# Kernel tuning notes

Measured on AMD Instinct MI355X. Metric: run time of the kernel, lower is better.

Reference implementation:

```python
import jax, jax.numpy as jnp
import numpy as np

B, T, D, FF, E = 4, 2048, 512, 2048, 8
TOP_K = 2
EPS = 0.01


def setup_inputs() -> dict:
    key = jax.random.key(0)
    ks = jax.random.split(key, 7)
    s = 0.02
    return {
        "x": jax.random.normal(ks[0], (B, T, D), dtype=jnp.float32),
        "Wg": jax.random.normal(ks[1], (D, E), dtype=jnp.float32) * s,
        "bg": jnp.zeros((E,), dtype=jnp.float32),
        "W1": jax.random.normal(ks[2], (E, D, FF), dtype=jnp.float32) * s,
        "b1": jnp.zeros((E, FF), dtype=jnp.float32),
        "W2": jax.random.normal(ks[3], (E, FF, D), dtype=jnp.float32) * s,
        "b2": jnp.zeros((E, D), dtype=jnp.float32),
    }


def reference(x, Wg, bg, W1, b1, W2, b2):
    b, t, d = x.shape
    e = Wg.shape[1]
    # Gating: softmax over experts, top-k selection, renormalize with eps.
    logits = jnp.einsum("btd,de->bte", x, Wg) + bg          # [B,T,E]
    gates = jax.nn.softmax(logits, axis=-1)
    vals, idx = jax.lax.top_k(gates, TOP_K)                  # [B,T,K]
    vals = vals / (jnp.sum(vals, axis=-1, keepdims=True) + EPS)
    # Per-token per-expert combine weight (scatter of top-k vals into E slots).
    w = jnp.sum(jax.nn.one_hot(idx, e, dtype=x.dtype) * vals[..., None], axis=-2)  # [B,T,E]
    w = w.reshape(-1, e)                                     # [N,E], N=B*T
    xf = x.reshape(-1, d)                                    # [N,D]
    # Per-expert FFN (Linear -> ReLU -> Linear); zero-weight tokens contribute 0,
    # matching the original's masked gather/scatter.
    h = jax.nn.relu(jnp.einsum("nd,edf->enf", xf, W1) + b1[:, None, :])  # [E,N,FF]
    y = jnp.einsum("enf,efd->end", h, W2) + b2[:, None, :]               # [E,N,D]
    out = jnp.einsum("ne,end->nd", w, y)                                 # [N,D]
    return out.reshape(b, t, d)
```

## Files before the change

kernel.cpp:

```cpp
#include <hip/hip_runtime.h>
#include <hip/hip_bf16.h>
#include <cstdint>

#define NTOK   8192
#define DDIM   512
#define FDIM   2048
#define NEXP   8
#define NSLOT  16384
#define MAXTILES 136

typedef __bf16 bf16;
typedef __bf16 bf16x8 __attribute__((ext_vector_type(8)));
typedef float  f32x4  __attribute__((ext_vector_type(4)));

typedef uint32_t __attribute__((address_space(1))) gu32;
typedef uint32_t __attribute__((address_space(3))) lu32;

__device__ __forceinline__ void gload16(const void* g, void* l) {
    __builtin_amdgcn_global_load_lds((const gu32*)(uintptr_t)g,
                                     (lu32*)(uintptr_t)l, 16, 0, 0);
}

__global__ __launch_bounds__(256)
void gating_kernel(const float* __restrict__ x, const float* __restrict__ Wg,
                   const float* __restrict__ bg, bf16* __restrict__ xb,
                   int* __restrict__ top_idx, float* __restrict__ top_w,
                   int* __restrict__ counts)
{
    __shared__ int cnt_s[NEXP];
    if (threadIdx.x < NEXP) cnt_s[threadIdx.x] = 0;
    __syncthreads();

    const int w = threadIdx.x >> 6;
    const int l = threadIdx.x & 63;
    const int gw = blockIdx.x * 4 + w;

    for (int n = gw; n < NTOK; n += 4096) {
        const float4* xp = (const float4*)(x + (size_t)n * DDIM + l * 8);
        float4 x0 = xp[0], x1 = xp[1];
        float xf[8] = {x0.x, x0.y, x0.z, x0.w, x1.x, x1.y, x1.z, x1.w};

        bf16x8 xv;
#pragma unroll
        for (int i = 0; i < 8; ++i) xv[i] = (bf16)xf[i];
        *(bf16x8*)(xb + (size_t)n * DDIM + l * 8) = xv;

        float acc[8] = {0.f,0.f,0.f,0.f,0.f,0.f,0.f,0.f};
#pragma unroll
        for (int i = 0; i < 8; ++i) {
            const float4* wp = (const float4*)(Wg + (size_t)(l * 8 + i) * NEXP);
            float4 wa = wp[0], wb = wp[1];
            acc[0] += xf[i] * wa.x; acc[1] += xf[i] * wa.y;
            acc[2] += xf[i] * wa.z; acc[3] += xf[i] * wa.w;
            acc[4] += xf[i] * wb.x; acc[5] += xf[i] * wb.y;
            acc[6] += xf[i] * wb.z; acc[7] += xf[i] * wb.w;
        }
#pragma unroll
        for (int m = 32; m >= 1; m >>= 1)
#pragma unroll
            for (int e = 0; e < 8; ++e)
                acc[e] += __shfl_xor(acc[e], m);

        if (l == 0) {
            float logit[8];
#pragma unroll
            for (int e = 0; e < 8; ++e) logit[e] = acc[e] + bg[e];
            float mx = logit[0];
#pragma unroll
            for (int e = 1; e < 8; ++e) mx = fmaxf(mx, logit[e]);
            float g[8], s = 0.f;
#pragma unroll
            for (int e = 0; e < 8; ++e) { g[e] = expf(logit[e] - mx); s += g[e]; }
            float inv = 1.f / s;
#pragma unroll
            for (int e = 0; e < 8; ++e) g[e] *= inv;
            int e0 = 0;
#pragma unroll
            for (int e = 1; e < 8; ++e) if (g[e] > g[e0]) e0 = e;
            int e1 = (e0 == 0) ? 1 : 0;
#pragma unroll
            for (int e = 0; e < 8; ++e) if (e != e0 && e != e1 && g[e] > g[e1]) e1 = e;
            float denom = g[e0] + g[e1] + 0.01f;
            top_idx[n * 2 + 0] = e0;
            top_idx[n * 2 + 1] = e1;
            top_w[n * 2 + 0] = g[e0] / denom;
            top_w[n * 2 + 1] = g[e1] / denom;
            atomicAdd(&cnt_s[e0], 1);
            atomicAdd(&cnt_s[e1], 1);
        }
    }
    __syncthreads();
    if (threadIdx.x < NEXP) atomicAdd(&counts[threadIdx.x], cnt_s[threadIdx.x]);
}

__global__ void scan_kernel(const int* __restrict__ counts, int* __restrict__ offsets,
                            int* __restrict__ tmap_e, int* __restrict__ tmap_rt,
                            int* __restrict__ ntiles, int* __restrict__ cursors)
{
    if (threadIdx.x == 0) {
        int off = 0;
        for (int e = 0; e < NEXP; ++e) { offsets[e] = off; off += counts[e]; cursors[e] = 0; }
        offsets[NEXP] = off;
        int t = 0;
        for (int e = 0; e < NEXP; ++e) {
            int nt = (counts[e] + 127) >> 7;
            for (int rt = 0; rt < nt; ++rt) { tmap_e[t] = e; tmap_rt[t] = rt; ++t; }
        }
        *ntiles = t;
    }
}

__global__ __launch_bounds__(256)
void scatter_kernel(const int* __restrict__ top_idx, const float* __restrict__ top_w,
                    const int* __restrict__ offsets, int* __restrict__ cursors,
                    int* __restrict__ slot_tok, float* __restrict__ slot_w,
                    int* __restrict__ pos)
{
    __shared__ int lcnt[NEXP];
    __shared__ int lbase[NEXP];
    const int t = threadIdx.x;
    if (t < NEXP) lcnt[t] = 0;
    __syncthreads();
    const int n = blockIdx.x * 256 + t;
    const int e0 = top_idx[n * 2 + 0];
    const int e1 = top_idx[n * 2 + 1];
    const int r0 = atomicAdd(&lcnt[e0], 1);
    const int r1 = atomicAdd(&lcnt[e1], 1);
    __syncthreads();
    if (t < NEXP) lbase[t] = atomicAdd(&cursors[t], lcnt[t]);
    __syncthreads();
    const int s0 = offsets[e0] + lbase[e0] + r0;
    const int s1 = offsets[e1] + lbase[e1] + r1;
    slot_tok[s0] = n; slot_w[s0] = top_w[n * 2 + 0]; pos[n * 2 + 0] = s0;
    slot_tok[s1] = n; slot_w[s1] = top_w[n * 2 + 1]; pos[n * 2 + 1] = s1;
}

__global__ __launch_bounds__(256)
void transpose_cvt(const float* __restrict__ src, bf16* __restrict__ dst, int R, int C)
{
    __shared__ bf16 tile[64][72];
    const size_t eo = (size_t)blockIdx.z * R * C;
    src += eo; dst += eo;
    const int c0 = blockIdx.x * 64, r0 = blockIdx.y * 64;
    const int tq = (threadIdx.x & 15) * 4;
    const int tr = threadIdx.x >> 4;
#pragma unroll
    for (int j = 0; j < 4; ++j) {
        const int r = tr + j * 16;
        float4 v = *(const float4*)(src + (size_t)(r0 + r) * C + c0 + tq);
        tile[tq + 0][r] = (bf16)v.x;
        tile[tq + 1][r] = (bf16)v.y;
        tile[tq + 2][r] = (bf16)v.z;
        tile[tq + 3][r] = (bf16)v.w;
    }
    __syncthreads();
    const int x8 = (threadIdx.x & 7) * 8;
    const int cr = threadIdx.x >> 3;
#pragma unroll
    for (int j = 0; j < 2; ++j) {
        const int c = cr + j * 32;
        *(bf16x8*)(dst + (size_t)(c0 + c) * R + r0 + x8) = *(const bf16x8*)&tile[c][x8];
    }
}

template<int KD, int ND, bool FIRST>
__global__ __launch_bounds__(512)
void moe_gemm(const bf16* __restrict__ Adata, const bf16* __restrict__ Bt,
              const float* __restrict__ bias, void* __restrict__ Out,
              const int* __restrict__ slot_tok, const int* __restrict__ offsets,
              const int* __restrict__ tmap_e, const int* __restrict__ tmap_rt,
              const int* __restrict__ ntiles)
{
    const int ty = blockIdx.y;
    if (ty >= *ntiles) return;
    const int e    = tmap_e[ty];
    const int rt   = tmap_rt[ty];
    const int row0 = offsets[e] + rt * 128;
    const int rowEnd = offsets[e + 1];
    const int nb   = blockIdx.x * 128;

    __shared__ __align__(16) bf16 As[4 * 128 * 32];
    __shared__ __align__(16) bf16 Bs[4 * 128 * 32];

    const int t = threadIdx.x;
    const int w = t >> 6, l = t & 63;
    const int wm = w >> 1, wn = w & 1;

    const int rA   = w * 16 + (l >> 2);
    const int colb = (l & 3) * 8;

    int srow = row0 + rA; if (srow >= NSLOT) srow = NSLOT - 1;
    const bf16* aSrc;
    if (FIRST) aSrc = Adata + (size_t)slot_tok[srow] * KD + colb;
    else       aSrc = Adata + (size_t)srow * KD + colb;
    const bf16* bSrc = Bt + ((size_t)e * ND + nb + rA) * KD + colb;

    const int offW = w * 512;

    f32x4 acc[2][4] = {};
    const int lr = l & 15;
    const int lk = (l >> 4) * 8;

    constexpr int NT = KD / 32;

    auto STAGE = [&](int buf, int k0) {
        gload16(aSrc + k0, As + buf * 4096 + offW);
        gload16(bSrc + k0, Bs + buf * 4096 + offW);
    };
    auto COMPUTE = [&](int buf) {
        const bf16* ab = As + buf * 4096;
        const bf16* bb = Bs + buf * 4096;
        bf16x8 aF[2], bF[4];
#pragma unroll
        for (int mi = 0; mi < 2; ++mi)
            aF[mi] = *(const bf16x8*)(ab + (wm * 32 + mi * 16 + lr) * 32 + lk);
#pragma unroll
        for (int nj = 0; nj < 4; ++nj)
            bF[nj] = *(const bf16x8*)(bb + (wn * 64 + nj * 16 + lr) * 32 + lk);
#pragma unroll
        for (int mi = 0; mi < 2; ++mi)
#pragma unroll
            for (int nj = 0; nj < 4; ++nj)
                acc[mi][nj] = __builtin_amdgcn_mfma_f32_16x16x32_bf16(
                    aF[mi], bF[nj], acc[mi][nj], 0, 0, 0);
    };

    STAGE(0, 0);
    STAGE(1, 32);
    STAGE(2, 64);
    STAGE(3, 96);
    __builtin_amdgcn_sched_barrier(0);

    for (int t2 = 0; t2 < NT - 4; ++t2) {
        asm volatile("s_waitcnt vmcnt(6)" ::: "memory");
        __builtin_amdgcn_sched_barrier(0);
        __builtin_amdgcn_s_barrier();
        __builtin_amdgcn_sched_barrier(0);
        COMPUTE(t2 & 3);
        __builtin_amdgcn_s_barrier();
        __builtin_amdgcn_sched_barrier(0);
        STAGE(t2 & 3, (t2 + 4) * 32);
        __builtin_amdgcn_sched_barrier(0);
    }
    asm volatile("s_waitcnt vmcnt(6)" ::: "memory");
    __builtin_amdgcn_sched_barrier(0);
    __builtin_amdgcn_s_barrier();
    __builtin_amdgcn_sched_barrier(0);
    COMPUTE((NT - 4) & 3);
    asm volatile("s_waitcnt vmcnt(4)" ::: "memory");
    __builtin_amdgcn_sched_barrier(0);
    __builtin_amdgcn_s_barrier();
    __builtin_amdgcn_sched_barrier(0);
    COMPUTE((NT - 3) & 3);
    asm volatile("s_waitcnt vmcnt(2)" ::: "memory");
    __builtin_amdgcn_sched_barrier(0);
    __builtin_amdgcn_s_barrier();
    __builtin_amdgcn_sched_barrier(0);
    COMPUTE((NT - 2) & 3);
    asm volatile("s_waitcnt vmcnt(0)" ::: "memory");
    __builtin_amdgcn_sched_barrier(0);
    __builtin_amdgcn_s_barrier();
    __builtin_amdgcn_sched_barrier(0);
    COMPUTE((NT - 1) & 3);

    const int rowW = row0 + wm * 32;
    const int colW = nb + wn * 64;
#pragma unroll
    for (int mi = 0; mi < 2; ++mi) {
#pragma unroll
        for (int nj = 0; nj < 4; ++nj) {
#pragma unroll
            for (int r = 0; r < 4; ++r) {
                int row = rowW + mi * 16 + (l >> 4) * 4 + r;
                int col = colW + nj * 16 + lr;
                if (row < rowEnd) {
                    float v = acc[mi][nj][r] + bias[e * ND + col];
                    if (FIRST)
                        ((bf16*)Out)[(size_t)row * ND + col] = (bf16)fmaxf(v, 0.f);
                    else
                        ((float*)Out)[(size_t)row * ND + col] = v;
                }
            }
        }
    }
}

__global__ __launch_bounds__(256)
void combine_kernel(const float* __restrict__ Yg, const int* __restrict__ pos,
                    const float* __restrict__ slot_w, float* __restrict__ out)
{
    int idx = blockIdx.x * 256 + threadIdx.x;
    int n = idx >> 7;
    int d4 = idx & 127;
    int s0 = pos[n * 2 + 0], s1 = pos[n * 2 + 1];
    float w0 = slot_w[s0], w1 = slot_w[s1];
    float4 a = ((const float4*)(Yg + (size_t)s0 * DDIM))[d4];
    float4 b = ((const float4*)(Yg + (size_t)s1 * DDIM))[d4];
    float4 o;
    o.x = w0 * a.x + w1 * b.x;
    o.y = w0 * a.y + w1 * b.y;
    o.z = w0 * a.z + w1 * b.z;
    o.w = w0 * a.w + w1 * b.w;
    ((float4*)out)[idx] = o;
}

extern "C" void kernel_launch(void* const* d_in, const int* in_sizes, int n_in,
                              void* d_out, int out_size, void* d_ws, size_t ws_size,
                              hipStream_t stream)
{
    (void)in_sizes; (void)n_in;
    const float* x  = (const float*)d_in[0];
    const float* Wg = (const float*)d_in[1];
    const float* bg = (const float*)d_in[2];
    const float* W1 = (const float*)d_in[3];
    const float* b1 = (const float*)d_in[4];
    const float* W2 = (const float*)d_in[5];
    const float* b2 = (const float*)d_in[6];
    float* out = (float*)d_out;

    uint8_t* ws = (uint8_t*)d_ws;
    size_t off = 0;
    auto alloc = [&](size_t bytes) -> void* {
        void* p = ws + off;
        off = (off + bytes + 255) & ~(size_t)255;
        return p;
    };
    bf16*  xb      = (bf16*)alloc((size_t)NTOK * DDIM * 2);
    bf16*  w1t     = (bf16*)alloc((size_t)NEXP * FDIM * DDIM * 2);
    bf16*  w2t     = (bf16*)alloc((size_t)NEXP * DDIM * FDIM * 2);
    bf16*  Hg      = (bf16*)alloc((size_t)NSLOT * FDIM * 2);
    float* Yg      = (float*)alloc((size_t)NSLOT * DDIM * 4);
    int*   counts  = (int*)alloc(NEXP * 4);
    int*   cursors = (int*)alloc(NEXP * 4);
    int*   offsets = (int*)alloc((NEXP + 1) * 4);
    int*   ntiles  = (int*)alloc(4);
    int*   tmap_e  = (int*)alloc(MAXTILES * 4);
    int*   tmap_rt = (int*)alloc(MAXTILES * 4);
    int*   top_idx = (int*)alloc((size_t)NTOK * 2 * 4);
    float* top_w   = (float*)alloc((size_t)NTOK * 2 * 4);
    int*   pos     = (int*)alloc((size_t)NTOK * 2 * 4);
    int*   slot_tok= (int*)alloc((size_t)NSLOT * 4);
    float* slot_w  = (float*)alloc((size_t)NSLOT * 4);

    if (ws_size < off) {
        hipMemsetAsync(d_out, 0, (size_t)out_size * 4, stream);
        return;
    }

    hipMemsetAsync(counts, 0, NEXP * 4, stream);

    gating_kernel<<<1024, 256, 0, stream>>>(x, Wg, bg, xb, top_idx, top_w, counts);
    scan_kernel<<<1, 64, 0, stream>>>(counts, offsets, tmap_e, tmap_rt, ntiles, cursors);
    scatter_kernel<<<NTOK / 256, 256, 0, stream>>>(top_idx, top_w, offsets, cursors,
                                                   slot_tok, slot_w, pos);
    transpose_cvt<<<dim3(FDIM / 64, DDIM / 64, NEXP), 256, 0, stream>>>(W1, w1t, DDIM, FDIM);
    transpose_cvt<<<dim3(DDIM / 64, FDIM / 64, NEXP), 256, 0, stream>>>(W2, w2t, FDIM, DDIM);

    moe_gemm<DDIM, FDIM, true><<<dim3(FDIM / 128, MAXTILES), 512, 0, stream>>>(
        xb, w1t, b1, (void*)Hg, slot_tok, offsets, tmap_e, tmap_rt, ntiles);
    moe_gemm<FDIM, DDIM, false><<<dim3(DDIM / 128, MAXTILES), 512, 0, stream>>>(
        Hg, w2t, b2, (void*)Yg, slot_tok, offsets, tmap_e, tmap_rt, ntiles);

    combine_kernel<<<(NTOK * DDIM / 4) / 256, 256, 0, stream>>>(Yg, pos, slot_w, out);
}
```

Before: 205.6 us.

## Remap workgroups across XCDs and shrink GEMM pipeline to three stages

Workgroup IDs are remapped so that consecutive work items land on the same XCD chiplet (round-robin by 8). Neighbouring tiles that share expert weights then hit the same L2. The LDS ring buffer drops from four stages to three, cutting shared memory per block from 64KB to 48KB so more blocks can be resident per CU. The trade-off is a shallower prefetch distance, which may expose more memory latency, and the remap assumes NWG divides evenly by 8.

```diff
diff --git a/kernel.cpp b/kernel.cpp
--- a/kernel.cpp
+++ b/kernel.cpp
@@ -171,16 +171,24 @@
               const int* __restrict__ tmap_e, const int* __restrict__ tmap_rt,
               const int* __restrict__ ntiles)
 {
-    const int ty = blockIdx.y;
-    if (ty >= *ntiles) return;
-    const int e    = tmap_e[ty];
-    const int rt   = tmap_rt[ty];
+    constexpr int NX  = ND / 128;
+    constexpr int NWG = NX * MAXTILES;
+    constexpr int Q   = NWG / 8;
+
+    const int orig = blockIdx.y * NX + blockIdx.x;
+    const int work = (orig & 7) * Q + (orig >> 3);
+    const int wy   = work / NX;
+    const int wx   = work - wy * NX;
+    if (wy >= *ntiles) return;
+
+    const int e    = tmap_e[wy];
+    const int rt   = tmap_rt[wy];
     const int row0 = offsets[e] + rt * 128;
     const int rowEnd = offsets[e + 1];
-    const int nb   = blockIdx.x * 128;
-
-    __shared__ __align__(16) bf16 As[4 * 128 * 32];
-    __shared__ __align__(16) bf16 Bs[4 * 128 * 32];
+    const int nb   = wx * 128;
+
+    __shared__ __align__(16) bf16 As[3 * 128 * 32];
+    __shared__ __align__(16) bf16 Bs[3 * 128 * 32];
 
     const int t = threadIdx.x;
     const int w = t >> 6, l = t & 63;
@@ -228,40 +236,38 @@
     STAGE(0, 0);
     STAGE(1, 32);
     STAGE(2, 64);
-    STAGE(3, 96);
-    __builtin_amdgcn_sched_barrier(0);
-
-    for (int t2 = 0; t2 < NT - 4; ++t2) {
-        asm volatile("s_waitcnt vmcnt(6)" ::: "memory");
+    __builtin_amdgcn_sched_barrier(0);
+
+    int buf = 0;
+    for (int t2 = 0; t2 < NT - 3; ++t2) {
+        asm volatile("s_waitcnt vmcnt(4)" ::: "memory");
         __builtin_amdgcn_sched_barrier(0);
         __builtin_amdgcn_s_barrier();
         __builtin_amdgcn_sched_barrier(0);
-        COMPUTE(t2 & 3);
+        COMPUTE(buf);
         __builtin_amdgcn_s_barrier();
         __builtin_amdgcn_sched_barrier(0);
-        STAGE(t2 & 3, (t2 + 4) * 32);
+        STAGE(buf, (t2 + 3) * 32);
         __builtin_amdgcn_sched_barrier(0);
-    }
-    asm volatile("s_waitcnt vmcnt(6)" ::: "memory");
+        buf = (buf == 2) ? 0 : buf + 1;
+    }
+    asm volatile("s_waitcnt vmcnt(4)" ::: "memory");
     __builtin_amdgcn_sched_barrier(0);
     __builtin_amdgcn_s_barrier();
     __builtin_amdgcn_sched_barrier(0);
-    COMPUTE((NT - 4) & 3);
-    asm volatile("s_waitcnt vmcnt(4)" ::: "memory");
+    COMPUTE(buf);
+    buf = (buf == 2) ? 0 : buf + 1;
+    asm volatile("s_waitcnt vmcnt(2)" ::: "memory");
     __builtin_amdgcn_sched_barrier(0);
     __builtin_amdgcn_s_barrier();
     __builtin_amdgcn_sched_barrier(0);
-    COMPUTE((NT - 3) & 3);
-    asm volatile("s_waitcnt vmcnt(2)" ::: "memory");
+    COMPUTE(buf);
+    buf = (buf == 2) ? 0 : buf + 1;
+    asm volatile("s_waitcnt vmcnt(0)" ::: "memory");
     __builtin_amdgcn_sched_barrier(0);
     __builtin_amdgcn_s_barrier();
     __builtin_amdgcn_sched_barrier(0);
-    COMPUTE((NT - 2) & 3);
-    asm volatile("s_waitcnt vmcnt(0)" ::: "memory");
-    __builtin_amdgcn_sched_barrier(0);
-    __builtin_amdgcn_s_barrier();
-    __builtin_amdgcn_sched_barrier(0);
-    COMPUTE((NT - 1) & 3);
+    COMPUTE(buf);
 
     const int rowW = row0 + wm * 32;
     const int colW = nb + wn * 64;
```

Result: faster. 184.5 us (-10.3%).
